# Optimization experiments

Measured on AMD Instinct MI355X. Metric: run time of the kernel, lower is better.

Reference implementation:

```python
import jax, jax.numpy as jnp
import numpy as np

B, N, H, L = 32, 64, 128, 4
EPS = 1e-5


def _fc_edges(batch, n):
    # fully-connected edges (no self loops), per graph, then offset per batch element
    idx = np.arange(n)
    rows = np.repeat(idx, n)
    cols = np.tile(idx, n)
    keep = rows != cols
    rows, cols = rows[keep], cols[keep]  # [n*(n-1)]
    offs = (np.arange(batch) * n)[:, None]
    row = (rows[None, :] + offs).reshape(-1)
    col = (cols[None, :] + offs).reshape(-1)
    return jnp.asarray(row, jnp.int32), jnp.asarray(col, jnp.int32)


def _layernorm(x, g, b):
    mu = jnp.mean(x, axis=-1, keepdims=True)
    var = jnp.var(x, axis=-1, keepdims=True)
    return (x - mu) * jax.lax.rsqrt(var + EPS) * g + b


def _gelu(x):
    return jax.nn.gelu(x, approximate=False)  # torch nn.GELU default (erf)


def setup_inputs() -> dict:
    key = jax.random.key(0)
    ks = jax.random.split(key, 10)
    s = 0.05
    return {
        "h": jax.random.normal(ks[0], (B * N, H), jnp.float32),
        "coord": jax.random.normal(ks[1], (B, N, 2), jnp.float32),
        "ln_g": jnp.ones((L, H), jnp.float32),
        "ln_b": jnp.zeros((L, H), jnp.float32),
        "cW1": jax.random.normal(ks[2], (L, 2, H), jnp.float32) * s,
        "cb1": jnp.zeros((L, H), jnp.float32),
        "cW2": jax.random.normal(ks[3], (L, H, H), jnp.float32) * s,
        "cb2": jnp.zeros((L, H), jnp.float32),
        "eW1": jax.random.normal(ks[4], (L, 3 * H, H), jnp.float32) * s,
        "eb1": jnp.zeros((L, H), jnp.float32),
        "eW2": jax.random.normal(ks[5], (L, H, H), jnp.float32) * s,
        "eb2": jnp.zeros((L, H), jnp.float32),
        "nW1": jax.random.normal(ks[6], (L, 2 * H, H), jnp.float32) * s,
        "nb1": jnp.zeros((L, H), jnp.float32),
        "nW2": jax.random.normal(ks[7], (L, H, H), jnp.float32) * s,
        "nb2": jnp.zeros((L, H), jnp.float32),
    }


def reference(h, coord, ln_g, ln_b, cW1, cb1, cW2, cb2,
              eW1, eb1, eW2, eb2, nW1, nb1, nW2, nb2):
    row, col = _fc_edges(B, N)
    coord_f = coord.reshape(B * N, 2)
    coord_diff = coord_f[row] - coord_f[col]  # [E, 2]
    for i in range(L):
        hn = _layernorm(h, ln_g[i], ln_b[i])  # [BN, H]
        # coord MLP on edge displacements
        cd = _gelu(coord_diff @ cW1[i] + cb1[i])
        cd = _gelu(cd @ cW2[i] + cb2[i])  # [E, H]
        # edge model: gather endpoints, concat, MLP
        ef = jnp.concatenate([hn[row], hn[col], cd], axis=1)  # [E, 3H]
        ef = _gelu(ef @ eW1[i] + eb1[i])
        ef = _gelu(ef @ eW2[i] + eb2[i])  # [E, H]
        # node model: scatter-add aggregation, concat, MLP, residual
        agg = jax.ops.segment_sum(ef, row, num_segments=B * N)  # [BN, H]
        out = _gelu(jnp.concatenate([hn, agg], axis=1) @ nW1[i] + nb1[i])
        out = out @ nW2[i] + nb2[i]
        h = hn + out  # residual on layer-normed h, as in torch code
    return h
```

## Files before the change

### kernel.cpp

```cpp
#include <hip/hip_runtime.h>
#include <math.h>

#define NN 64
#define HH 128
#define LL 4

#define OFF_CW2T 0
#define OFF_W1AT 16384
#define OFF_W1BT 32768
#define OFF_W1CT 49152
#define OFF_EW2T 65536
#define OFF_NW2T 81920
#define OFF_NW1T 98304
#define WT_LAYER 131072

typedef short s8v __attribute__((ext_vector_type(8)));
typedef float f4v __attribute__((ext_vector_type(4)));

__device__ __forceinline__ short f2bf(float f){
  unsigned u = __float_as_uint(f);
  u += 0x7fffu + ((u>>16)&1u);
  return (short)(u>>16);
}
__device__ __forceinline__ float gelu(float x){
  float z = fabsf(x) * 0.70710678118654752f;
  float t = __builtin_amdgcn_rcpf(fmaf(0.3275911f, z, 1.0f));
  float p = fmaf(fmaf(fmaf(fmaf(1.061405429f, t, -1.453152027f), t,
                 1.421413741f), t, -0.284496736f), t, 0.254829592f) * t;
  float e = __expf(-z*z);
  float er = 1.0f - p*e;
  er = copysignf(er, x);
  return 0.5f*x*(1.0f+er);
}
__device__ __forceinline__ f4v mfma16(s8v a, s8v b, f4v c){
  return __builtin_amdgcn_mfma_f32_16x16x32_bf16(a,b,c,0,0,0);
}

__global__ __launch_bounds__(256) void k_wt(
  const float* __restrict__ cW2, const float* __restrict__ eW1,
  const float* __restrict__ eW2, const float* __restrict__ nW1,
  const float* __restrict__ nW2, short* __restrict__ WT)
{
  int gid = blockIdx.x*256 + threadIdx.x;
  int l = gid >> 17;
  int r = gid & 131071;
  float v;
  if (r < 32768 && r >= 16384){
    int i = r-16384; int n = i>>7, k = i&127;
    v = eW1[l*49152 + k*128 + n];
  } else if (r < 16384){
    int n = r>>7, k = r&127;
    v = cW2[l*16384 + k*128 + n];
  } else if (r < 49152){
    int i = r-32768; int n = i>>7, k = i&127;
    v = eW1[l*49152 + (128+k)*128 + n];
  } else if (r < 65536){
    int i = r-49152; int n = i>>7, k = i&127;
    v = eW1[l*49152 + (256+k)*128 + n];
  } else if (r < 81920){
    int i = r-65536; int n = i>>7, k = i&127;
    v = eW2[l*16384 + k*128 + n];
  } else if (r < 98304){
    int i = r-81920; int n = i>>7, k = i&127;
    v = nW2[l*16384 + k*128 + n];
  } else {
    int i = r-98304; int n = i>>8, k = i&255;
    v = nW1[l*32768 + k*128 + n];
  }
  WT[gid] = f2bf(v);
}

__global__ __launch_bounds__(256) void k_ln_ab(
    const float* __restrict__ h,
    const float* __restrict__ lng, const float* __restrict__ lnb,
    const short* __restrict__ WT,
    float* __restrict__ hnf, float* __restrict__ ABf)
{
  __shared__ __align__(16) short hl[16*128];
  const int t = threadIdx.x;
  const int nl = t>>4, l16 = t&15;
  const int gn = blockIdx.x*16 + nl;
  const float* hp = h + gn*128 + l16*8;
  float4 f0 = *(const float4*)hp;
  float4 f1 = *(const float4*)(hp+4);
  float x[8] = {f0.x,f0.y,f0.z,f0.w,f1.x,f1.y,f1.z,f1.w};
  float s=0.f, sq=0.f;
  #pragma unroll
  for (int i=0;i<8;i++){ s += x[i]; sq += x[i]*x[i]; }
  #pragma unroll
  for (int m=1;m<16;m<<=1){ s += __shfl_xor(s,m,64); sq += __shfl_xor(sq,m,64); }
  float mu = s*(1.f/128.f);
  float var = sq*(1.f/128.f) - mu*mu;
  float rstd = rsqrtf(var + 1e-5f);
  s8v pk;
  float y[8];
  #pragma unroll
  for (int i=0;i<8;i++){
    int k = l16*8+i;
    y[i] = (x[i]-mu)*rstd*lng[k] + lnb[k];
    pk[i] = f2bf(y[i]);
  }
  float4 o0; o0.x=y[0];o0.y=y[1];o0.z=y[2];o0.w=y[3];
  float4 o1; o1.x=y[4];o1.y=y[5];o1.z=y[6];o1.w=y[7];
  *(float4*)(hnf + gn*128 + l16*8)     = o0;
  *(float4*)(hnf + gn*128 + l16*8 + 4) = o1;
  *(s8v*)&hl[nl*128 + ((l16 ^ (nl&7))<<3)] = pk;
  __syncthreads();

  const int w = t>>6, lane = t&63, q = lane>>4, c16 = lane&15;
  f4v acc[4];
  #pragma unroll
  for (int j=0;j<4;j++){
    #pragma unroll
    for (int e=0;e<4;e++) acc[j][e] = 0.f;
  }
  #pragma unroll
  for (int s4=0;s4<4;s4++){
    int kc = 4*s4+q;
    s8v a = *(const s8v*)&hl[c16*128 + ((kc ^ (c16&7))<<3)];
    #pragma unroll
    for (int j=0;j<4;j++){
      int cn = (w*4+j)*16 + c16;
      const short* bp = (cn < 128) ? (WT + OFF_W1AT + cn*128)
                                   : (WT + OFF_W1BT + (cn-128)*128);
      s8v bb = *(const s8v*)(bp + kc*8);
      acc[j] = mfma16(a, bb, acc[j]);
    }
  }
  #pragma unroll
  for (int j=0;j<4;j++){
    int cn = (w*4+j)*16 + c16;
    #pragma unroll
    for (int r=0;r<4;r++){
      ABf[(blockIdx.x*16 + 4*q + r)*256 + cn] = acc[j][r];
    }
  }
}

__global__ __launch_bounds__(512, 2) void k_edge(
    const float* __restrict__ coord,
    const float* __restrict__ cW1l,
    const float* __restrict__ cb1g, const float* __restrict__ cb2g,
    const float* __restrict__ eb1g, const float* __restrict__ eb2g,
    const short* __restrict__ WT,
    const float* __restrict__ ABf,
    float* __restrict__ agg)
{
  __shared__ __align__(16) short Wc[2*128*128];
  __shared__ __align__(16) short t0[64*128];
  __shared__ __align__(16) short t1[64*128];
  __shared__ __align__(16) float Atf[8*128];
  __shared__ __align__(16) float Btf[64*128];
  __shared__ __align__(16) float aggl[8*128];
  __shared__ float w1x[128], w1y[128], b1s[128], b2s[128], e1s[128], e2s[128];
  __shared__ float cxr[8], cyr[8], cxj[64], cyj[64];

  const int t = threadIdx.x;
  const int b  = blockIdx.x >> 3;
  const int rb = blockIdx.x & 7;
  const int gbase = b*NN;
  const int rows0 = gbase + rb*8;

  #pragma unroll
  for (int i=0;i<4;i++){
    int idx16 = t + i*512;
    int n = idx16>>4, c = idx16&15;
    int dsw = n*128 + ((c ^ (n&7))<<3);
    *(s8v*)&Wc[dsw]          = *(const s8v*)(WT + OFF_CW2T + n*128 + c*8);
    *(s8v*)&Wc[16384 + dsw]  = *(const s8v*)(WT + OFF_EW2T + n*128 + c*8);
  }
  if (t < 128){
    w1x[t] = cW1l[t]; w1y[t] = cW1l[128+t];
    b1s[t] = cb1g[t]; b2s[t] = cb2g[t];
    e1s[t] = eb1g[t]; e2s[t] = eb2g[t];
  }
  if (t < 64){ cxj[t] = coord[(gbase+t)*2]; cyj[t] = coord[(gbase+t)*2+1]; }
  if (t >= 64 && t < 72){ int r=t-64; cxr[r] = coord[(rows0+r)*2]; cyr[r] = coord[(rows0+r)*2+1]; }
  if (t < 256){
    int r = t>>5, c = t&31;
    *(float4*)&Atf[r*128 + c*4] = *(const float4*)(ABf + (rows0+r)*256 + c*4);
  }
  #pragma unroll
  for (int i=0;i<4;i++){
    int idx4 = t + i*512;
    int j = idx4>>5, c = idx4&31;
    *(float4*)&Btf[j*128 + c*4] = *(const float4*)(ABf + (gbase+j)*256 + 128 + c*4);
  }
  #pragma unroll
  for (int i=0;i<2;i++) aggl[t + i*512] = 0.f;

  const int w = t>>6, lane = t&63, q = lane>>4, c16 = lane&15;
  const int mt  = w>>1;
  const int ntb = (w&1)*4;

  s8v wreg[4][4];
  #pragma unroll
  for (int j=0;j<4;j++){
    int n = (ntb+j)*16 + c16;
    #pragma unroll
    for (int s=0;s<4;s++)
      wreg[j][s] = *(const s8v*)(WT + OFF_W1CT + n*128 + (4*s+q)*8);
  }
  __syncthreads();

  const int row0 = mt*16 + c16;
  const int swz  = row0 & 7;

  for (int ch=0; ch<8; ch++){
    const int j0 = ch*8;
    {
      int m = t & 63;
      int r = m>>3, jj = m&7;
      float dx = cxr[r] - cxj[j0+jj];
      float dy = cyr[r] - cyj[j0+jj];
      int cb0 = t>>6;
      #pragma unroll
      for (int hf=0; hf<2; hf++){
        int kc = cb0 + hf*8;
        s8v pk;
        #pragma unroll
        for (int kk=0;kk<8;kk++){
          int k = kc*8+kk;
          pk[kk] = f2bf(gelu(fmaf(dx, w1x[k], fmaf(dy, w1y[k], b1s[k]))));
        }
        *(s8v*)&t0[m*128 + ((kc ^ (m&7))<<3)] = pk;
      }
    }
    __syncthreads();
    {
      f4v acc[4];
      #pragma unroll
      for (int j=0;j<4;j++){
        #pragma unroll
        for (int e=0;e<4;e++) acc[j][e]=0.f;
      }
      #pragma unroll
      for (int s=0;s<4;s++){
        int kc = 4*s+q;
        s8v a0 = *(const s8v*)&t0[row0*128 + ((kc ^ swz)<<3)];
        #pragma unroll
        for (int j=0;j<4;j++){
          int n = (ntb+j)*16 + c16;
          s8v bb = *(const s8v*)&Wc[n*128 + ((kc ^ (n&7))<<3)];
          acc[j] = mfma16(a0, bb, acc[j]);
        }
      }
      #pragma unroll
      for (int j=0;j<4;j++){
        int cn = (ntb+j)*16 + c16;
        #pragma unroll
        for (int r=0;r<4;r++){
          int m = mt*16 + 4*q + r;
          float v = acc[j][r] + b2s[cn];
          t1[m*128 + (((cn>>3) ^ (m&7))<<3) + (cn&7)] = f2bf(gelu(v));
        }
      }
    }
    __syncthreads();
    {
      f4v acc[4];
      #pragma unroll
      for (int j=0;j<4;j++){
        #pragma unroll
        for (int e=0;e<4;e++) acc[j][e]=0.f;
      }
      #pragma unroll
      for (int s=0;s<4;s++){
        int kc = 4*s+q;
        s8v a0 = *(const s8v*)&t1[row0*128 + ((kc ^ swz)<<3)];
        #pragma unroll
        for (int j=0;j<4;j++)
          acc[j] = mfma16(a0, wreg[j][s], acc[j]);
      }
      #pragma unroll
      for (int j=0;j<4;j++){
        int cn = (ntb+j)*16 + c16;
        #pragma unroll
        for (int r=0;r<4;r++){
          int m = mt*16 + 4*q + r;
          int rr = m>>3, jj = m&7;
          float v = acc[j][r] + Atf[rr*128+cn] + Btf[(j0+jj)*128+cn] + e1s[cn];
          t0[m*128 + (((cn>>3) ^ (m&7))<<3) + (cn&7)] = f2bf(gelu(v));
        }
      }
    }
    __syncthreads();
    {
      f4v acc[4];
      #pragma unroll
      for (int j=0;j<4;j++){
        #pragma unroll
        for (int e=0;e<4;e++) acc[j][e]=0.f;
      }
      #pragma unroll
      for (int s=0;s<4;s++){
        int kc = 4*s+q;
        s8v a0 = *(const s8v*)&t0[row0*128 + ((kc ^ swz)<<3)];
        #pragma unroll
        for (int j=0;j<4;j++){
          int n = (ntb+j)*16 + c16;
          s8v bb = *(const s8v*)&Wc[16384 + n*128 + ((kc ^ (n&7))<<3)];
          acc[j] = mfma16(a0, bb, acc[j]);
        }
      }
      #pragma unroll
      for (int j=0;j<4;j++){
        int cn = (ntb+j)*16 + c16;
        float s = 0.f;
        #pragma unroll
        for (int r=0;r<4;r++){
          int m = mt*16 + 4*q + r;
          float g = gelu(acc[j][r] + e2s[cn]);
          int rr = m>>3, jj = m&7;
          if (rb*8 + rr == j0 + jj) g = 0.f;
          s += g;
        }
        s += __shfl_xor(s, 16, 64);
        if ((q&1)==0)
          aggl[(2*mt + (q>>1))*128 + cn] += s;
      }
    }
    __syncthreads();
  }
  #pragma unroll
  for (int i=0;i<2;i++){
    int idx = t + i*512;
    agg[(rows0 + (idx>>7))*128 + (idx&127)] = aggl[idx];
  }
}

__global__ __launch_bounds__(256) void k_node(
    const float* __restrict__ hnf, const float* __restrict__ aggg,
    const float* __restrict__ nb1l, const float* __restrict__ nb2l,
    const short* __restrict__ WT,
    float* __restrict__ hout)
{
  __shared__ __align__(16) short cat[16*256];
  __shared__ __align__(16) short u1[16*128];
  __shared__ __align__(16) float hf[16*128];
  const int t = threadIdx.x;
  {
    const int row = t>>4, c = t&15;
    const int gn = blockIdx.x*16 + row;
    float4 f0 = *(const float4*)(hnf + gn*128 + c*8);
    float4 f1 = *(const float4*)(hnf + gn*128 + c*8 + 4);
    *(float4*)&hf[row*128 + c*8]     = f0;
    *(float4*)&hf[row*128 + c*8 + 4] = f1;
    s8v p;
    p[0]=f2bf(f0.x);p[1]=f2bf(f0.y);p[2]=f2bf(f0.z);p[3]=f2bf(f0.w);
    p[4]=f2bf(f1.x);p[5]=f2bf(f1.y);p[6]=f2bf(f1.z);p[7]=f2bf(f1.w);
    *(s8v*)&cat[row*256 + ((c ^ (row&7))<<3)] = p;
    float4 g0 = *(const float4*)(aggg + gn*128 + c*8);
    float4 g1 = *(const float4*)(aggg + gn*128 + c*8 + 4);
    s8v pg;
    pg[0]=f2bf(g0.x);pg[1]=f2bf(g0.y);pg[2]=f2bf(g0.z);pg[3]=f2bf(g0.w);
    pg[4]=f2bf(g1.x);pg[5]=f2bf(g1.y);pg[6]=f2bf(g1.z);pg[7]=f2bf(g1.w);
    *(s8v*)&cat[row*256 + (((16+c) ^ (row&7))<<3)] = pg;
  }
  __syncthreads();
  const int w = t>>6, lane = t&63, q = lane>>4, c16 = lane&15;
  f4v acc[2];
  #pragma unroll
  for (int j=0;j<2;j++){
    #pragma unroll
    for (int e=0;e<4;e++) acc[j][e]=0.f;
  }
  #pragma unroll
  for (int s=0;s<8;s++){
    int kc = 4*s+q;
    s8v a = *(const s8v*)&cat[c16*256 + ((kc ^ (c16&7))<<3)];
    #pragma unroll
    for (int j=0;j<2;j++){
      int cn = (w*2+j)*16 + c16;
      s8v bb = *(const s8v*)(WT + OFF_NW1T + cn*256 + kc*8);
      acc[j] = mfma16(a, bb, acc[j]);
    }
  }
  #pragma unroll
  for (int j=0;j<2;j++){
    int cn = (w*2+j)*16 + c16;
    #pragma unroll
    for (int r=0;r<4;r++){
      int m = 4*q+r;
      float v = acc[j][r] + nb1l[cn];
      u1[m*128 + (((cn>>3) ^ (m&7))<<3) + (cn&7)] = f2bf(gelu(v));
    }
  }
  __syncthreads();
  f4v acc2[2];
  #pragma unroll
  for (int j=0;j<2;j++){
    #pragma unroll
    for (int e=0;e<4;e++) acc2[j][e]=0.f;
  }
  #pragma unroll
  for (int s=0;s<4;s++){
    int kc = 4*s+q;
    s8v a = *(const s8v*)&u1[c16*128 + ((kc ^ (c16&7))<<3)];
    #pragma unroll
    for (int j=0;j<2;j++){
      int cn = (w*2+j)*16 + c16;
      s8v bb = *(const s8v*)(WT + OFF_NW2T + cn*128 + kc*8);
      acc2[j] = mfma16(a, bb, acc2[j]);
    }
  }
  #pragma unroll
  for (int j=0;j<2;j++){
    int cn = (w*2+j)*16 + c16;
    #pragma unroll
    for (int r=0;r<4;r++){
      int m = 4*q+r;
      hout[(blockIdx.x*16 + m)*128 + cn] = hf[m*128 + cn] + acc2[j][r] + nb2l[cn];
    }
  }
}

__global__ __launch_bounds__(256) void k_node_ln(
    const float* hnf, const float* __restrict__ aggg,
    const float* __restrict__ nb1l, const float* __restrict__ nb2l,
    const short* __restrict__ WTl,
    const float* __restrict__ lng, const float* __restrict__ lnb,
    const short* __restrict__ WTn,
    float* hnf_out, float* __restrict__ ABf)
{
  __shared__ __align__(16) short cat[16*256];
  __shared__ __align__(16) short u1[16*128];
  __shared__ __align__(16) float hf[16*128];
  __shared__ __align__(16) float hnw[16*128];
  __shared__ __align__(16) short hl[16*128];
  const int t = threadIdx.x;
  {
    const int row = t>>4, c = t&15;
    const int gn = blockIdx.x*16 + row;
    float4 f0 = *(const float4*)(hnf + gn*128 + c*8);
    float4 f1 = *(const float4*)(hnf + gn*128 + c*8 + 4);
    *(float4*)&hf[row*128 + c*8]     = f0;
    *(float4*)&hf[row*128 + c*8 + 4] = f1;
    s8v p;
    p[0]=f2bf(f0.x);p[1]=f2bf(f0.y);p[2]=f2bf(f0.z);p[3]=f2bf(f0.w);
    p[4]=f2bf(f1.x);p[5]=f2bf(f1.y);p[6]=f2bf(f1.z);p[7]=f2bf(f1.w);
    *(s8v*)&cat[row*256 + ((c ^ (row&7))<<3)] = p;
    float4 g0 = *(const float4*)(aggg + gn*128 + c*8);
    float4 g1 = *(const float4*)(aggg + gn*128 + c*8 + 4);
    s8v pg;
    pg[0]=f2bf(g0.x);pg[1]=f2bf(g0.y);pg[2]=f2bf(g0.z);pg[3]=f2bf(g0.w);
    pg[4]=f2bf(g1.x);pg[5]=f2bf(g1.y);pg[6]=f2bf(g1.z);pg[7]=f2bf(g1.w);
    *(s8v*)&cat[row*256 + (((16+c) ^ (row&7))<<3)] = pg;
  }
  __syncthreads();
  const int w = t>>6, lane = t&63, q = lane>>4, c16 = lane&15;
  f4v acc[2];
  #pragma unroll
  for (int j=0;j<2;j++){
    #pragma unroll
    for (int e=0;e<4;e++) acc[j][e]=0.f;
  }
  #pragma unroll
  for (int s=0;s<8;s++){
    int kc = 4*s+q;
    s8v a = *(const s8v*)&cat[c16*256 + ((kc ^ (c16&7))<<3)];
    #pragma unroll
    for (int j=0;j<2;j++){
      int cn = (w*2+j)*16 + c16;
      s8v bb = *(const s8v*)(WTl + OFF_NW1T + cn*256 + kc*8);
      acc[j] = mfma16(a, bb, acc[j]);
    }
  }
  #pragma unroll
  for (int j=0;j<2;j++){
    int cn = (w*2+j)*16 + c16;
    #pragma unroll
    for (int r=0;r<4;r++){
      int m = 4*q+r;
      float v = acc[j][r] + nb1l[cn];
      u1[m*128 + (((cn>>3) ^ (m&7))<<3) + (cn&7)] = f2bf(gelu(v));
    }
  }
  __syncthreads();
  f4v acc2[2];
  #pragma unroll
  for (int j=0;j<2;j++){
    #pragma unroll
    for (int e=0;e<4;e++) acc2[j][e]=0.f;
  }
  #pragma unroll
  for (int s=0;s<4;s++){
    int kc = 4*s+q;
    s8v a = *(const s8v*)&u1[c16*128 + ((kc ^ (c16&7))<<3)];
    #pragma unroll
    for (int j=0;j<2;j++){
      int cn = (w*2+j)*16 + c16;
      s8v bb = *(const s8v*)(WTn ? (WTl + OFF_NW2T + cn*128 + kc*8)
                                 : (WTl + OFF_NW2T + cn*128 + kc*8));
      acc2[j] = mfma16(a, bb, acc2[j]);
    }
  }
  #pragma unroll
  for (int j=0;j<2;j++){
    int cn = (w*2+j)*16 + c16;
    #pragma unroll
    for (int r=0;r<4;r++){
      int m = 4*q+r;
      hnw[m*128 + cn] = hf[m*128 + cn] + acc2[j][r] + nb2l[cn];
    }
  }
  __syncthreads();
  {
    const int nl = t>>4, l16 = t&15;
    const int gn = blockIdx.x*16 + nl;
    float x[8];
    #pragma unroll
    for (int i=0;i<8;i++) x[i] = hnw[nl*128 + l16*8 + i];
    float s=0.f, sq=0.f;
    #pragma unroll
    for (int i=0;i<8;i++){ s += x[i]; sq += x[i]*x[i]; }
    #pragma unroll
    for (int m=1;m<16;m<<=1){ s += __shfl_xor(s,m,64); sq += __shfl_xor(sq,m,64); }
    float mu = s*(1.f/128.f);
    float var = sq*(1.f/128.f) - mu*mu;
    float rstd = rsqrtf(var + 1e-5f);
    s8v pk;
    float y[8];
    #pragma unroll
    for (int i=0;i<8;i++){
      int k = l16*8+i;
      y[i] = (x[i]-mu)*rstd*lng[k] + lnb[k];
      pk[i] = f2bf(y[i]);
    }
    float4 o0; o0.x=y[0];o0.y=y[1];o0.z=y[2];o0.w=y[3];
    float4 o1; o1.x=y[4];o1.y=y[5];o1.z=y[6];o1.w=y[7];
    *(float4*)(hnf_out + gn*128 + l16*8)     = o0;
    *(float4*)(hnf_out + gn*128 + l16*8 + 4) = o1;
    *(s8v*)&hl[nl*128 + ((l16 ^ (nl&7))<<3)] = pk;
  }
  __syncthreads();
  f4v accab[4];
  #pragma unroll
  for (int j=0;j<4;j++){
    #pragma unroll
    for (int e=0;e<4;e++) accab[j][e] = 0.f;
  }
  #pragma unroll
  for (int s4=0;s4<4;s4++){
    int kc = 4*s4+q;
    s8v a = *(const s8v*)&hl[c16*128 + ((kc ^ (c16&7))<<3)];
    #pragma unroll
    for (int j=0;j<4;j++){
      int cn = (w*4+j)*16 + c16;
      const short* bp = (cn < 128) ? (WTn + OFF_W1AT + cn*128)
                                   : (WTn + OFF_W1BT + (cn-128)*128);
      s8v bb = *(const s8v*)(bp + kc*8);
      accab[j] = mfma16(a, bb, accab[j]);
    }
  }
  #pragma unroll
  for (int j=0;j<4;j++){
    int cn = (w*4+j)*16 + c16;
    #pragma unroll
    for (int r=0;r<4;r++){
      ABf[(blockIdx.x*16 + 4*q + r)*256 + cn] = accab[j][r];
    }
  }
}

extern "C" void kernel_launch(void* const* d_in, const int* in_sizes, int n_in,
                              void* d_out, int out_size, void* d_ws, size_t ws_size,
                              hipStream_t stream)
{
  (void)in_sizes; (void)n_in; (void)out_size; (void)ws_size;
  const float* h     = (const float*)d_in[0];
  const float* coord = (const float*)d_in[1];
  const float* ln_g  = (const float*)d_in[2];
  const float* ln_b  = (const float*)d_in[3];
  const float* cW1   = (const float*)d_in[4];
  const float* cb1   = (const float*)d_in[5];
  const float* cW2   = (const float*)d_in[6];
  const float* cb2   = (const float*)d_in[7];
  const float* eW1   = (const float*)d_in[8];
  const float* eb1   = (const float*)d_in[9];
  const float* eW2   = (const float*)d_in[10];
  const float* eb2   = (const float*)d_in[11];
  const float* nW1   = (const float*)d_in[12];
  const float* nb1   = (const float*)d_in[13];
  const float* nW2   = (const float*)d_in[14];
  const float* nb2   = (const float*)d_in[15];

  char* ws = (char*)d_ws;
  short* WT   = (short*)(ws);
  float* hnf  = (float*)(ws + (1u<<20));
  float* ABf  = (float*)(ws + (2u<<20));
  float* aggf = (float*)(ws + (4u<<20));

  k_wt<<<2048, 256, 0, stream>>>(cW2, eW1, eW2, nW1, nW2, WT);
  k_ln_ab<<<128, 256, 0, stream>>>(h, ln_g, ln_b, WT, hnf, ABf);

  for (int l=0;l<LL;l++){
    const short* WTl = WT + l*WT_LAYER;
    k_edge<<<256, 512, 0, stream>>>(coord, cW1 + l*2*HH, cb1 + l*HH, cb2 + l*HH,
                                    eb1 + l*HH, eb2 + l*HH, WTl, ABf, aggf);
    if (l < LL-1){
      const short* WTn = WT + (l+1)*WT_LAYER;
      k_node_ln<<<128, 256, 0, stream>>>(hnf, aggf, nb1 + l*HH, nb2 + l*HH, WTl,
                                         ln_g + (l+1)*HH, ln_b + (l+1)*HH, WTn,
                                         hnf, ABf);
    } else {
      k_node<<<128, 256, 0, stream>>>(hnf, aggf, nb1 + l*HH, nb2 + l*HH, WTl,
                                      (float*)d_out);
    }
  }
}
```

Before: 368.8 us.

## Restructure edge kernel so each wave owns one source row, removing block barriers

```diff
diff --git a/kernel.cpp b/kernel.cpp
--- a/kernel.cpp
+++ b/kernel.cpp
@@ -147,19 +147,15 @@
     float* __restrict__ agg)
 {
   __shared__ __align__(16) short Wc[2*128*128];
-  __shared__ __align__(16) short t0[64*128];
-  __shared__ __align__(16) short t1[64*128];
-  __shared__ __align__(16) float Atf[8*128];
-  __shared__ __align__(16) float Btf[64*128];
-  __shared__ __align__(16) float aggl[8*128];
-  __shared__ float w1x[128], w1y[128], b1s[128], b2s[128], e1s[128], e2s[128];
-  __shared__ float cxr[8], cyr[8], cxj[64], cyj[64];
+  __shared__ __align__(16) short T[128*128];
+  __shared__ __align__(16) float Btf[64*132];
+  __shared__ float w1x[128], w1y[128], b1s[128], b2s[128], e2s[128];
+  __shared__ float cxj[64], cyj[64];
 
   const int t = threadIdx.x;
   const int b  = blockIdx.x >> 3;
   const int rb = blockIdx.x & 7;
   const int gbase = b*NN;
-  const int rows0 = gbase + rb*8;
 
   #pragma unroll
   for (int i=0;i<4;i++){
@@ -171,161 +167,151 @@
   }
   if (t < 128){
     w1x[t] = cW1l[t]; w1y[t] = cW1l[128+t];
-    b1s[t] = cb1g[t]; b2s[t] = cb2g[t];
-    e1s[t] = eb1g[t]; e2s[t] = eb2g[t];
-  }
-  if (t < 64){ cxj[t] = coord[(gbase+t)*2]; cyj[t] = coord[(gbase+t)*2+1]; }
-  if (t >= 64 && t < 72){ int r=t-64; cxr[r] = coord[(rows0+r)*2]; cyr[r] = coord[(rows0+r)*2+1]; }
-  if (t < 256){
-    int r = t>>5, c = t&31;
-    *(float4*)&Atf[r*128 + c*4] = *(const float4*)(ABf + (rows0+r)*256 + c*4);
+    b1s[t] = cb1g[t]; b2s[t] = cb2g[t]; e2s[t] = eb2g[t];
+  }
+  if (t >= 128 && t < 192){
+    int j = t-128;
+    cxj[j] = coord[(gbase+j)*2]; cyj[j] = coord[(gbase+j)*2+1];
   }
   #pragma unroll
   for (int i=0;i<4;i++){
     int idx4 = t + i*512;
     int j = idx4>>5, c = idx4&31;
-    *(float4*)&Btf[j*128 + c*4] = *(const float4*)(ABf + (gbase+j)*256 + 128 + c*4);
-  }
-  #pragma unroll
-  for (int i=0;i<2;i++) aggl[t + i*512] = 0.f;
+    *(float4*)&Btf[j*132 + c*4] = *(const float4*)(ABf + (gbase+j)*256 + 128 + c*4);
+  }
 
   const int w = t>>6, lane = t&63, q = lane>>4, c16 = lane&15;
-  const int mt  = w>>1;
-  const int ntb = (w&1)*4;
-
-  s8v wreg[4][4];
-  #pragma unroll
-  for (int j=0;j<4;j++){
-    int n = (ntb+j)*16 + c16;
+  const int rg = rb*8 + w;
+
+  s8v wreg[8][4];
+  #pragma unroll
+  for (int j=0;j<8;j++){
+    int n = j*16 + c16;
     #pragma unroll
     for (int s=0;s<4;s++)
       wreg[j][s] = *(const s8v*)(WT + OFF_W1CT + n*128 + (4*s+q)*8);
   }
-  __syncthreads();
-
-  const int row0 = mt*16 + c16;
-  const int swz  = row0 & 7;
-
-  for (int ch=0; ch<8; ch++){
-    const int j0 = ch*8;
-    {
-      int m = t & 63;
-      int r = m>>3, jj = m&7;
-      float dx = cxr[r] - cxj[j0+jj];
-      float dy = cyr[r] - cyj[j0+jj];
-      int cb0 = t>>6;
-      #pragma unroll
-      for (int hf=0; hf<2; hf++){
-        int kc = cb0 + hf*8;
-        s8v pk;
-        #pragma unroll
-        for (int kk=0;kk<8;kk++){
-          int k = kc*8+kk;
-          pk[kk] = f2bf(gelu(fmaf(dx, w1x[k], fmaf(dy, w1y[k], b1s[k]))));
-        }
-        *(s8v*)&t0[m*128 + ((kc ^ (m&7))<<3)] = pk;
+  float atf[8];
+  #pragma unroll
+  for (int j=0;j<8;j++){
+    int cn = j*16 + c16;
+    atf[j] = ABf[(gbase+rg)*256 + cn] + eb1g[cn];
+  }
+  float aggreg[8];
+  #pragma unroll
+  for (int j=0;j<8;j++) aggreg[j]=0.f;
+
+  __syncthreads();
+
+  const float cx_r = cxj[rg];
+  const float cy_r = cyj[rg];
+  const int rowA = w*16 + c16;
+  const int swzA = rowA & 7;
+
+  for (int ch=0; ch<4; ch++){
+    const int j0 = ch*16;
+    float dx = cx_r - cxj[j0 + c16];
+    float dy = cy_r - cyj[j0 + c16];
+    s8v afr[4];
+    #pragma unroll
+    for (int s=0;s<4;s++){
+      #pragma unroll
+      for (int kk=0;kk<8;kk++){
+        int k = (4*s+q)*8 + kk;
+        afr[s][kk] = f2bf(gelu(fmaf(dx, w1x[k], fmaf(dy, w1y[k], b1s[k]))));
       }
     }
-    __syncthreads();
-    {
-      f4v acc[4];
-      #pragma unroll
-      for (int j=0;j<4;j++){
-        #pragma unroll
-        for (int e=0;e<4;e++) acc[j][e]=0.f;
+    f4v acc[8];
+    #pragma unroll
+    for (int j=0;j<8;j++){
+      #pragma unroll
+      for (int e=0;e<4;e++) acc[j][e]=0.f;
+    }
+    #pragma unroll
+    for (int s=0;s<4;s++){
+      int kc = 4*s+q;
+      #pragma unroll
+      for (int j=0;j<8;j++){
+        int n = j*16 + c16;
+        s8v bb = *(const s8v*)&Wc[n*128 + ((kc ^ (n&7))<<3)];
+        acc[j] = mfma16(afr[s], bb, acc[j]);
       }
-      #pragma unroll
-      for (int s=0;s<4;s++){
-        int kc = 4*s+q;
-        s8v a0 = *(const s8v*)&t0[row0*128 + ((kc ^ swz)<<3)];
-        #pragma unroll
-        for (int j=0;j<4;j++){
-          int n = (ntb+j)*16 + c16;
-          s8v bb = *(const s8v*)&Wc[n*128 + ((kc ^ (n&7))<<3)];
-          acc[j] = mfma16(a0, bb, acc[j]);
-        }
+    }
+    #pragma unroll
+    for (int j=0;j<8;j++){
+      int cn = j*16 + c16;
+      #pragma unroll
+      for (int r=0;r<4;r++){
+        int m = w*16 + 4*q + r;
+        float v = acc[j][r] + b2s[cn];
+        T[m*128 + (((cn>>3) ^ (m&7))<<3) + (cn&7)] = f2bf(gelu(v));
       }
-      #pragma unroll
-      for (int j=0;j<4;j++){
-        int cn = (ntb+j)*16 + c16;
-        #pragma unroll
-        for (int r=0;r<4;r++){
-          int m = mt*16 + 4*q + r;
-          float v = acc[j][r] + b2s[cn];
-          t1[m*128 + (((cn>>3) ^ (m&7))<<3) + (cn&7)] = f2bf(gelu(v));
-        }
+    }
+    s8v afc[4];
+    #pragma unroll
+    for (int s=0;s<4;s++)
+      afc[s] = *(const s8v*)&T[rowA*128 + (((4*s+q) ^ swzA)<<3)];
+    #pragma unroll
+    for (int j=0;j<8;j++){
+      #pragma unroll
+      for (int e=0;e<4;e++) acc[j][e]=0.f;
+    }
+    #pragma unroll
+    for (int s=0;s<4;s++){
+      #pragma unroll
+      for (int j=0;j<8;j++)
+        acc[j] = mfma16(afc[s], wreg[j][s], acc[j]);
+    }
+    #pragma unroll
+    for (int j=0;j<8;j++){
+      int cn = j*16 + c16;
+      #pragma unroll
+      for (int r=0;r<4;r++){
+        int m = w*16 + 4*q + r;
+        int jj = 4*q + r;
+        float v = acc[j][r] + atf[j] + Btf[(j0+jj)*132 + cn];
+        T[m*128 + (((cn>>3) ^ (m&7))<<3) + (cn&7)] = f2bf(gelu(v));
       }
     }
-    __syncthreads();
-    {
-      f4v acc[4];
-      #pragma unroll
-      for (int j=0;j<4;j++){
-        #pragma unroll
-        for (int e=0;e<4;e++) acc[j][e]=0.f;
+    s8v afd[4];
+    #pragma unroll
+    for (int s=0;s<4;s++)
+      afd[s] = *(const s8v*)&T[rowA*128 + (((4*s+q) ^ swzA)<<3)];
+    #pragma unroll
+    for (int j=0;j<8;j++){
+      #pragma unroll
+      for (int e=0;e<4;e++) acc[j][e]=0.f;
+    }
+    #pragma unroll
+    for (int s=0;s<4;s++){
+      int kc = 4*s+q;
+      #pragma unroll
+      for (int j=0;j<8;j++){
+        int n = j*16 + c16;
+        s8v bb = *(const s8v*)&Wc[16384 + n*128 + ((kc ^ (n&7))<<3)];
+        acc[j] = mfma16(afd[s], bb, acc[j]);
       }
-      #pragma unroll
-      for (int s=0;s<4;s++){
-        int kc = 4*s+q;
-        s8v a0 = *(const s8v*)&t1[row0*128 + ((kc ^ swz)<<3)];
-        #pragma unroll
-        for (int j=0;j<4;j++)
-          acc[j] = mfma16(a0, wreg[j][s], acc[j]);
+    }
+    #pragma unroll
+    for (int j=0;j<8;j++){
+      int cn = j*16 + c16;
+      float ssum = 0.f;
+      #pragma unroll
+      for (int r=0;r<4;r++){
+        int jj = 4*q + r;
+        float g = gelu(acc[j][r] + e2s[cn]);
+        if (rg == j0 + jj) g = 0.f;
+        ssum += g;
       }
-      #pragma unroll
-      for (int j=0;j<4;j++){
-        int cn = (ntb+j)*16 + c16;
-        #pragma unroll
-        for (int r=0;r<4;r++){
-          int m = mt*16 + 4*q + r;
-          int rr = m>>3, jj = m&7;
-          float v = acc[j][r] + Atf[rr*128+cn] + Btf[(j0+jj)*128+cn] + e1s[cn];
-          t0[m*128 + (((cn>>3) ^ (m&7))<<3) + (cn&7)] = f2bf(gelu(v));
-        }
-      }
-    }
-    __syncthreads();
-    {
-      f4v acc[4];
-      #pragma unroll
-      for (int j=0;j<4;j++){
-        #pragma unroll
-        for (int e=0;e<4;e++) acc[j][e]=0.f;
-      }
-      #pragma unroll
-      for (int s=0;s<4;s++){
-        int kc = 4*s+q;
-        s8v a0 = *(const s8v*)&t0[row0*128 + ((kc ^ swz)<<3)];
-        #pragma unroll
-        for (int j=0;j<4;j++){
-          int n = (ntb+j)*16 + c16;
-          s8v bb = *(const s8v*)&Wc[16384 + n*128 + ((kc ^ (n&7))<<3)];
-          acc[j] = mfma16(a0, bb, acc[j]);
-        }
-      }
-      #pragma unroll
-      for (int j=0;j<4;j++){
-        int cn = (ntb+j)*16 + c16;
-        float s = 0.f;
-        #pragma unroll
-        for (int r=0;r<4;r++){
-          int m = mt*16 + 4*q + r;
-          float g = gelu(acc[j][r] + e2s[cn]);
-          int rr = m>>3, jj = m&7;
-          if (rb*8 + rr == j0 + jj) g = 0.f;
-          s += g;
-        }
-        s += __shfl_xor(s, 16, 64);
-        if ((q&1)==0)
-          aggl[(2*mt + (q>>1))*128 + cn] += s;
-      }
-    }
-    __syncthreads();
-  }
-  #pragma unroll
-  for (int i=0;i<2;i++){
-    int idx = t + i*512;
-    agg[(rows0 + (idx>>7))*128 + (idx&127)] = aggl[idx];
+      aggreg[j] += ssum;
+    }
+  }
+  #pragma unroll
+  for (int j=0;j<8;j++){
+    float v = aggreg[j];
+    v += __shfl_xor(v, 16, 64);
+    v += __shfl_xor(v, 32, 64);
+    if (q == 0) agg[(gbase+rg)*128 + j*16 + c16] = v;
   }
 }
 
@@ -490,8 +476,7 @@
     #pragma unroll
     for (int j=0;j<2;j++){
       int cn = (w*2+j)*16 + c16;
-      s8v bb = *(const s8v*)(WTn ? (WTl + OFF_NW2T + cn*128 + kc*8)
-                                 : (WTl + OFF_NW2T + cn*128 + kc*8));
+      s8v bb = *(const s8v*)(WTl + OFF_NW2T + cn*128 + kc*8);
       acc2[j] = mfma16(a, bb, acc2[j]);
     }
   }
```

Measured after the change: 624.3 us. 1.69x slower.
